# Kernel optimization log

Hardware: AMD Instinct MI355X
Metric: run time of the kernel (lower is better)

Reference implementation:

```python
import jax, jax.numpy as jnp
import numpy as np

B, L, SIZE, BACK, H = 4, 1024, 1024, 512, 16
D = SIZE // H  # head_size = 64


def setup_inputs() -> dict:
    key = jax.random.key(0)
    ks = jax.random.split(key, 18)
    s = 0.02
    return {
        "k": jax.random.normal(ks[0], (B, L, SIZE), jnp.float32),
        "v": jax.random.normal(ks[1], (B, L, SIZE), jnp.float32),
        "q": jax.random.normal(ks[2], (B, L, SIZE), jnp.float32),
        "background": jax.random.normal(ks[3], (B, L, BACK), jnp.float32),
        # weights stored [in, out] (pre-transposed vs torch Linear)
        "Wk": jax.random.normal(ks[4], (SIZE, SIZE), jnp.float32) * s,
        "bk": jnp.zeros((SIZE,), jnp.float32),
        "Wv": jax.random.normal(ks[5], (SIZE, SIZE), jnp.float32) * s,
        "bv": jnp.zeros((SIZE,), jnp.float32),
        "Wq": jax.random.normal(ks[6], (SIZE, SIZE), jnp.float32) * s,
        "bq": jnp.zeros((SIZE,), jnp.float32),
        "Wb": jax.random.normal(ks[7], (BACK, SIZE), jnp.float32) * s,
        "bb": jnp.zeros((SIZE,), jnp.float32),
        "Wo": jax.random.normal(ks[8], (SIZE, SIZE), jnp.float32) * s,
        "bo": jnp.zeros((SIZE,), jnp.float32),
    }


def _heads(x):
    # [B, L, H*D] -> [B, H, L, D]
    b, l, _ = x.shape
    return x.reshape(b, l, H, D).transpose(0, 2, 1, 3)


def reference(k, v, q, background, Wk, bk, Wv, bv, Wq, bq, Wb, bb, Wo, bo):
    kh = _heads(k @ Wk + bk)
    vh = _heads(v @ Wv + bv)
    qh = _heads(q @ Wq + bq) / jnp.sqrt(jnp.asarray(D, k.dtype))
    gh = _heads(background @ Wb + bb)
    scores = jnp.einsum("bhqd,bhkd->bhqk", qh, kh)   # [B,H,Lq,Lk]
    gates = jax.nn.sigmoid(jnp.einsum("bhqd,bhkd->bhqk", qh, gh))
    attn = jax.nn.softmax(scores, axis=-1) * gates    # dropout = identity (eval)
    ctx = jnp.einsum("bhqk,bhkd->bhqd", attn, vh)
    ctx = ctx.transpose(0, 2, 1, 3).reshape(k.shape[0], -1, H * D)
    return ctx @ Wo + bo
```

## Files before the change

### kernel.cpp

```cpp
#include <hip/hip_runtime.h>
#include <cstddef>
#include <cstdint>

typedef __attribute__((ext_vector_type(8))) short s16x8;
typedef __attribute__((ext_vector_type(4))) short s16x4;
typedef __attribute__((ext_vector_type(4))) float f32x4;

#define MFMA(a, b, c) __builtin_amdgcn_mfma_f32_16x16x32_bf16(a, b, c, 0, 0, 0)
#define LOG2E 1.44269504088896f

__device__ __forceinline__ short f2bf(float x) {
    uint32_t u = __float_as_uint(x);
    u = (u + 0x7FFFu + ((u >> 16) & 1u)) >> 16;
    return (short)u;
}

__device__ __forceinline__ void gld16(const void* g, void* l) {
    __builtin_amdgcn_global_load_lds(
        (const __attribute__((address_space(1))) unsigned int*)g,
        (__attribute__((address_space(3))) unsigned int*)l, 16, 0, 0);
}

__device__ __forceinline__ float fexp2(float x) {
#if __has_builtin(__builtin_amdgcn_exp2f)
    return __builtin_amdgcn_exp2f(x);
#else
    return exp2f(x);
#endif
}

__device__ __forceinline__ float frcp(float x) {
#if __has_builtin(__builtin_amdgcn_rcpf)
    return __builtin_amdgcn_rcpf(x);
#else
    return 1.f / x;
#endif
}

__device__ __forceinline__ unsigned cvtpk(float lo, float hi) {
    unsigned r;
    asm("v_cvt_pk_bf16_f32 %0, %1, %2" : "=v"(r) : "v"(lo), "v"(hi));
    return r;
}

struct ConvP { const float* in[4]; short* out[4]; };

__global__ __launch_bounds__(256)
void conv_all(ConvP p) {
    const int i = blockIdx.x * 256 + threadIdx.x;
    int r, base;
    if (i < 524288)            { r = 0; base = 0; }
    else if (i < 1048576)      { r = 1; base = 524288; }
    else if (i < 1310720)      { r = 2; base = 1048576; }
    else                       { r = 3; base = 1310720; }
    const int j = i - base;
    const float4 a = *(const float4*)(p.in[r] + (size_t)j * 8);
    const float4 b = *(const float4*)(p.in[r] + (size_t)j * 8 + 4);
    s16x8 o;
    o[0] = f2bf(a.x); o[1] = f2bf(a.y); o[2] = f2bf(a.z); o[3] = f2bf(a.w);
    o[4] = f2bf(b.x); o[5] = f2bf(b.y); o[6] = f2bf(b.z); o[7] = f2bf(b.w);
    *(s16x8*)(p.out[r] + (size_t)j * 8) = o;
}

struct WtP { const float* W[5]; short* Wt[5]; int K[5]; };

__global__ __launch_bounds__(256)
void conv_wt_b(WtP p) {
    __shared__ float T[64][65];
    const int z = blockIdx.z;
    const int K = p.K[z];
    const int k0 = blockIdx.y << 6, n0 = blockIdx.x << 6;
    if (k0 >= K) return;
    const float* W = p.W[z];
    short* Wt = p.Wt[z];
    const int tr = threadIdx.x >> 4, tc4 = (threadIdx.x & 15) << 2;
    #pragma unroll
    for (int i = 0; i < 4; ++i) {
        const int r = tr + i * 16;
        const float4 v = *(const float4*)(W + (size_t)(k0 + r) * 1024 + n0 + tc4);
        T[r][tc4 + 0] = v.x; T[r][tc4 + 1] = v.y;
        T[r][tc4 + 2] = v.z; T[r][tc4 + 3] = v.w;
    }
    __syncthreads();
    #pragma unroll
    for (int i = 0; i < 4; ++i) {
        const int nr = tr + i * 16;
        s16x4 o;
        o[0] = f2bf(T[tc4 + 0][nr]); o[1] = f2bf(T[tc4 + 1][nr]);
        o[2] = f2bf(T[tc4 + 2][nr]); o[3] = f2bf(T[tc4 + 3][nr]);
        *(s16x4*)(Wt + (size_t)(n0 + nr) * K + k0 + tc4) = o;
    }
}

struct Proj5P {
    const short* A[5]; const short* Bt[5]; const float* bias[5];
    void* Y[5]; int Kd[5]; float alpha[5]; int mode[5];
};

__global__ __launch_bounds__(256, 2)
void proj_gemm128d(Proj5P p, int zbase) {
    __shared__ __align__(16) short lds[2 * 16384];

    const int tid = threadIdx.x;
    const int w = tid >> 6, lane = tid & 63;
    const int la = lane & 15, kg = lane >> 4;
    const int wr = w >> 1, wc = w & 1;

    const int cpx = gridDim.x >> 3;
    const int orig = blockIdx.x;
    const int swz = (orig & 7) * cpx + (orig >> 3);
    const int z = zbase + (swz >> 8);
    const int rem = swz & 255;
    const int bm = rem >> 3, bn = rem & 7;

    const short* __restrict__ A  = p.A[z];
    const short* __restrict__ Bt = p.Bt[z];
    const int K = p.Kd[z];
    const int NT = K >> 6;

    const int srow = tid >> 3;
    const int csrc = (tid & 7) ^ (srow & 7);
    const short* gA = A  + (size_t)(bm * 128 + srow) * K + csrc * 8;
    const short* gB = Bt + (size_t)(bn * 128 + srow) * K + csrc * 8;
    short* dstA = &lds[srow * 64 + (tid & 7) * 8];
    short* dstB = dstA + 8192;

#define STAGE(t, nb) do {                                                  \
        const size_t ko_ = (size_t)((t) << 6);                             \
        short* ba_ = dstA + (nb) * 16384;                                  \
        short* bb_ = dstB + (nb) * 16384;                                  \
        _Pragma("unroll")                                                  \
        for (int i = 0; i < 4; ++i) {                                      \
            gld16(gA + (size_t)(32 * i) * K + ko_, ba_ + i * 2048);        \
            gld16(gB + (size_t)(32 * i) * K + ko_, bb_ + i * 2048);       \
        }                                                                  \
    } while (0)

    const int c0 = kg ^ (la & 7), c1 = (4 + kg) ^ (la & 7);
    const int aRd = (wr * 64 + la) * 64;
    const int bRd = 8192 + (wc * 64 + la) * 64;

    f32x4 acc[4][4] = {};

    STAGE(0, 0);
    asm volatile("s_waitcnt vmcnt(0)" ::: "memory");
    asm volatile("s_barrier" ::: "memory");

    for (int t = 0; t < NT; ++t) {
        const int cb = (t & 1) * 16384;
        if (t + 1 < NT) STAGE(t + 1, (t & 1) ^ 1);
        s16x8 af[4][2], bf[4][2];
        #pragma unroll
        for (int m = 0; m < 4; ++m) {
            af[m][0] = *(const s16x8*)&lds[cb + aRd + m * 1024 + c0 * 8];
            af[m][1] = *(const s16x8*)&lds[cb + aRd + m * 1024 + c1 * 8];
        }
        #pragma unroll
        for (int n = 0; n < 4; ++n) {
            bf[n][0] = *(const s16x8*)&lds[cb + bRd + n * 1024 + c0 * 8];
            bf[n][1] = *(const s16x8*)&lds[cb + bRd + n * 1024 + c1 * 8];
        }
        __builtin_amdgcn_s_setprio(1);
        #pragma unroll
        for (int m = 0; m < 4; ++m)
            #pragma unroll
            for (int n = 0; n < 4; ++n) {
                acc[m][n] = MFMA(af[m][0], bf[n][0], acc[m][n]);
                acc[m][n] = MFMA(af[m][1], bf[n][1], acc[m][n]);
            }
        __builtin_amdgcn_s_setprio(0);
        if (t + 1 < NT) {
            asm volatile("s_waitcnt vmcnt(0)" ::: "memory");
            asm volatile("s_barrier" ::: "memory");
        }
    }
#undef STAGE

    const float* __restrict__ bias = p.bias[z];
    const float alpha = p.alpha[z];
    const int mode = p.mode[z];

    if (mode == 2) {
        short* __restrict__ Y = (short*)p.Y[z];
        short* Tv = lds;
        asm volatile("s_waitcnt lgkmcnt(0)" ::: "memory");
        asm volatile("s_barrier" ::: "memory");
        #pragma unroll
        for (int ni = 0; ni < 4; ++ni) {
            const int rrow = wc * 64 + ni * 16 + la;
            const float bs = bias[bn * 128 + rrow];
            #pragma unroll
            for (int mi = 0; mi < 4; ++mi) {
                const int l0 = wr * 64 + mi * 16 + kg * 4;
                const unsigned d0 = cvtpk(alpha * (acc[mi][ni][0] + bs),
                                          alpha * (acc[mi][ni][1] + bs));
                const unsigned d1 = cvtpk(alpha * (acc[mi][ni][2] + bs),
                                          alpha * (acc[mi][ni][3] + bs));
                *(unsigned*)&Tv[rrow * 132 + l0]     = d0;
                *(unsigned*)&Tv[rrow * 132 + l0 + 2] = d1;
            }
        }
        asm volatile("s_barrier" ::: "memory");
        const int bb_ = (bm * 128) >> 10;
        const int l0g = (bm * 128) & 1023;
        #pragma unroll
        for (int s = 0; s < 8; ++s) {
            const int c = tid + (s << 8);
            const int rr = c >> 4, seg = c & 15;
            const int hh = bn * 2 + (rr >> 6), dd = rr & 63;
            const s16x8 vv = *(const s16x8*)&Tv[rr * 132 + seg * 8];
            *(s16x8*)&Y[((((size_t)bb_ * 16 + hh) * 64 + dd) << 10) + l0g + seg * 8] = vv;
        }
        return;
    }

    #pragma unroll
    for (int n = 0; n < 4; ++n) {
        const int col = bn * 128 + wc * 64 + n * 16 + la;
        const float bs = bias[col];
        #pragma unroll
        for (int m = 0; m < 4; ++m) {
            const int row0 = bm * 128 + wr * 64 + m * 16 + kg * 4;
            #pragma unroll
            for (int r = 0; r < 4; ++r) {
                const float v = alpha * (acc[m][n][r] + bs);
                if (mode == 0) {
                    ((short*)p.Y[z])[(size_t)(row0 + r) * 1024 + col] = f2bf(v);
                } else {
                    ((float*)p.Y[z])[(size_t)(row0 + r) * 1024 + col] = v;
                }
            }
        }
    }
}

__global__ __launch_bounds__(256)
void attn_mfma(const short* __restrict__ qh, const short* __restrict__ kh,
               const short* __restrict__ gh, const short* __restrict__ vt,
               short* __restrict__ ctx) {
    __shared__ __align__(16) short Ks[64 * 64];
    __shared__ __align__(16) short Gs[64 * 64];
    __shared__ __align__(16) short Vs[64 * 64];
    __shared__ __align__(16) short Ps[4][16 * 72];

    const int tid = threadIdx.x, w = tid >> 6, lane = tid & 63;
    const int la = lane & 15, kg = lane >> 4;
    const int q0 = blockIdx.x << 6;
    const int b = blockIdx.y >> 4, h = blockIdx.y & 15;
    const size_t hb = ((size_t)b << 20) + ((size_t)h << 6);
    const size_t vtbase = ((size_t)(b * 16 + h)) << 16;

    const int qrow = q0 + w * 16 + la;
    const s16x8 aq0 = *(const s16x8*)(qh + hb + (size_t)qrow * 1024 + kg * 8);
    const s16x8 aq1 = *(const s16x8*)(qh + hb + (size_t)qrow * 1024 + 32 + kg * 8);

    const int rl = lane >> 3;
    const int cs = (lane & 7) ^ rl;
    const size_t kgoff = hb + (size_t)(w * 8 + rl) * 1024 + cs * 8;
    const size_t vgoff = vtbase + (size_t)(w * 8 + rl) * 1024 + cs * 8;
    short* ldK0 = &Ks[(w * 8) * 64];      short* ldK1 = &Ks[(32 + w * 8) * 64];
    short* ldG0 = &Gs[(w * 8) * 64];      short* ldG1 = &Gs[(32 + w * 8) * 64];
    short* ldV0 = &Vs[(w * 8) * 64];      short* ldV1 = &Vs[(32 + w * 8) * 64];

    const int ch0 = (kg ^ (la & 7)) * 8;
    const int ch1 = ((4 + kg) ^ (la & 7)) * 8;

    float s_run = 0.f;
    f32x4 o[4] = {};

    for (int kt = 0; kt < 16; ++kt) {
        const size_t k0 = (size_t)(kt << 6);
        __syncthreads();
        gld16(kh + kgoff + k0 * 1024, ldK0);
        gld16(kh + kgoff + (k0 + 32) * 1024, ldK1);
        gld16(gh + kgoff + k0 * 1024, ldG0);
        gld16(gh + kgoff + (k0 + 32) * 1024, ldG1);
        gld16(vt + vgoff + k0, ldV0);
        gld16(vt + vgoff + 32 * 1024 + k0, ldV1);
        __syncthreads();

        f32x4 st[4] = {}, gt[4] = {};
        #pragma unroll
        for (int nf = 0; nf < 4; ++nf) {
            const int rb = (nf * 16 + la) * 64;
            const s16x8 kb0 = *(const s16x8*)&Ks[rb + ch0];
            const s16x8 kb1 = *(const s16x8*)&Ks[rb + ch1];
            st[nf] = MFMA(kb0, aq0, st[nf]);
            st[nf] = MFMA(kb1, aq1, st[nf]);
            const s16x8 gb0 = *(const s16x8*)&Gs[rb + ch0];
            const s16x8 gb1 = *(const s16x8*)&Gs[rb + ch1];
            gt[nf] = MFMA(gb0, aq0, gt[nf]);
            gt[nf] = MFMA(gb1, aq1, gt[nf]);
        }

        float ps = 0.f;
        unsigned pkw[4][2];
        #pragma unroll
        for (int nf = 0; nf < 4; ++nf) {
            const float p0 = fexp2(st[nf][0]);
            const float p1 = fexp2(st[nf][1]);
            const float p2 = fexp2(st[nf][2]);
            const float p3 = fexp2(st[nf][3]);
            ps += (p0 + p1) + (p2 + p3);
            const float g0 = frcp(1.f + fexp2(-gt[nf][0]));
            const float g1 = frcp(1.f + fexp2(-gt[nf][1]));
            const float g2 = frcp(1.f + fexp2(-gt[nf][2]));
            const float g3 = frcp(1.f + fexp2(-gt[nf][3]));
            pkw[nf][0] = cvtpk(p0 * g0, p1 * g1);
            pkw[nf][1] = cvtpk(p2 * g2, p3 * g3);
        }
        s_run += ps;

        #pragma unroll
        for (int nf = 0; nf < 4; ++nf) {
            *(unsigned*)&Ps[w][la * 72 + nf * 16 + kg * 4]     = pkw[nf][0];
            *(unsigned*)&Ps[w][la * 72 + nf * 16 + kg * 4 + 2] = pkw[nf][1];
        }

        const s16x8 pa0 = *(const s16x8*)&Ps[w][la * 72 + kg * 8];
        const s16x8 pa1 = *(const s16x8*)&Ps[w][la * 72 + 32 + kg * 8];
        #pragma unroll
        for (int nf = 0; nf < 4; ++nf) {
            const int rb = (nf * 16 + la) * 64;
            const s16x8 vb0 = *(const s16x8*)&Vs[rb + ch0];
            const s16x8 vb1 = *(const s16x8*)&Vs[rb + ch1];
            o[nf] = MFMA(vb0, pa0, o[nf]);
            o[nf] = MFMA(vb1, pa1, o[nf]);
        }
    }

    float sv = s_run;
    sv += __shfl_xor(sv, 16);
    sv += __shfl_xor(sv, 32);
    const float inv = frcp(sv);
    short* crow = ctx + ((size_t)(b * 1024 + qrow) << 10) + (h << 6);
    #pragma unroll
    for (int nf = 0; nf < 4; ++nf) {
        *(unsigned*)(crow + nf * 16 + kg * 4)     = cvtpk(o[nf][0] * inv, o[nf][1] * inv);
        *(unsigned*)(crow + nf * 16 + kg * 4 + 2) = cvtpk(o[nf][2] * inv, o[nf][3] * inv);
    }
}

extern "C" void kernel_launch(void* const* d_in, const int* in_sizes, int n_in,
                              void* d_out, int out_size, void* d_ws, size_t ws_size,
                              hipStream_t stream) {
    (void)in_sizes; (void)n_in; (void)out_size; (void)ws_size;

    const float* k  = (const float*)d_in[0];
    const float* v  = (const float*)d_in[1];
    const float* q  = (const float*)d_in[2];
    const float* bg = (const float*)d_in[3];
    const float* Wk = (const float*)d_in[4];  const float* bk = (const float*)d_in[5];
    const float* Wv = (const float*)d_in[6];  const float* bv = (const float*)d_in[7];
    const float* Wq = (const float*)d_in[8];  const float* bq = (const float*)d_in[9];
    const float* Wb = (const float*)d_in[10]; const float* bb = (const float*)d_in[11];
    const float* Wo = (const float*)d_in[12]; const float* bo = (const float*)d_in[13];

    short* ws = (short*)d_ws;
    const size_t MN = (size_t)4096 * 1024;
    short* khb = ws;
    short* qhb = ws + MN;
    short* ghb = ws + 2 * MN;
    short* vtb = ws + 3 * MN;
    short* xk  = ws + 4 * MN;
    short* xq  = ws + 5 * MN;
    short* xg  = ws + 6 * MN;
    short* xv  = ws + 6 * MN + MN / 2;
    short* wkt = ws + 7 * MN + MN / 2;
    short* wvt = wkt + 1048576;
    short* wqt = wvt + 1048576;
    short* wot = wqt + 1048576;
    short* wbt = wot + 1048576;
    short* ctxb = xk;

    const dim3 blk(256);

    WtP wp;
    wp.W[0] = Wk; wp.Wt[0] = wkt; wp.K[0] = 1024;
    wp.W[1] = Wv; wp.Wt[1] = wvt; wp.K[1] = 1024;
    wp.W[2] = Wq; wp.Wt[2] = wqt; wp.K[2] = 1024;
    wp.W[3] = Wb; wp.Wt[3] = wbt; wp.K[3] = 512;
    wp.W[4] = Wo; wp.Wt[4] = wot; wp.K[4] = 1024;
    conv_wt_b<<<dim3(16, 16, 5), blk, 0, stream>>>(wp);

    ConvP cp;
    cp.in[0] = k;  cp.out[0] = xk;
    cp.in[1] = q;  cp.out[1] = xq;
    cp.in[2] = bg; cp.out[2] = xg;
    cp.in[3] = v;  cp.out[3] = xv;
    conv_all<<<7168, blk, 0, stream>>>(cp);

    Proj5P p5;
    p5.A[0] = xk;   p5.Bt[0] = wkt; p5.bias[0] = bk; p5.Y[0] = khb;
    p5.Kd[0] = 1024; p5.alpha[0] = LOG2E;  p5.mode[0] = 0;
    p5.A[1] = xq;   p5.Bt[1] = wqt; p5.bias[1] = bq; p5.Y[1] = qhb;
    p5.Kd[1] = 1024; p5.alpha[1] = 0.125f; p5.mode[1] = 0;
    p5.A[2] = xg;   p5.Bt[2] = wbt; p5.bias[2] = bb; p5.Y[2] = ghb;
    p5.Kd[2] = 512;  p5.alpha[2] = LOG2E;  p5.mode[2] = 0;
    p5.A[3] = xv;   p5.Bt[3] = wvt; p5.bias[3] = bv; p5.Y[3] = vtb;
    p5.Kd[3] = 1024; p5.alpha[3] = 1.0f;   p5.mode[3] = 2;
    p5.A[4] = ctxb; p5.Bt[4] = wot; p5.bias[4] = bo; p5.Y[4] = d_out;
    p5.Kd[4] = 1024; p5.alpha[4] = 1.0f;   p5.mode[4] = 1;

    proj_gemm128d<<<dim3(1024), blk, 0, stream>>>(p5, 0);

    attn_mfma<<<dim3(16, 64), blk, 0, stream>>>(qhb, khb, ghb, vtb, ctxb);

    proj_gemm128d<<<dim3(256), blk, 0, stream>>>(p5, 4);
}
```

Before: 126.4 us.

## Double-buffer attention K/G/V tiles with 512-thread blocks and XCD-aware mapping

The attention kernel now uses 512-thread blocks that each cover 128 query rows, so every staged K/G/V tile is shared by twice as many waves. K, G and V tiles are double-buffered in one unified LDS array, and the next tile's global-to-LDS loads are issued before the current tile's compute, with one wait and barrier per iteration instead of two syncthreads. Blocks are remapped so each XCD handles contiguous batch-head groups, which should improve L2 locality. The costs are more LDS per block (about 66KB) and lower block-level occupancy.

```diff
diff --git a/kernel.cpp b/kernel.cpp
--- a/kernel.cpp
+++ b/kernel.cpp
@@ -234,61 +234,68 @@
     }
 }
 
-__global__ __launch_bounds__(256)
+__global__ __launch_bounds__(512)
 void attn_mfma(const short* __restrict__ qh, const short* __restrict__ kh,
                const short* __restrict__ gh, const short* __restrict__ vt,
                short* __restrict__ ctx) {
-    __shared__ __align__(16) short Ks[64 * 64];
-    __shared__ __align__(16) short Gs[64 * 64];
-    __shared__ __align__(16) short Vs[64 * 64];
-    __shared__ __align__(16) short Ps[4][16 * 72];
+    __shared__ __align__(16) short lds[33792];
 
     const int tid = threadIdx.x, w = tid >> 6, lane = tid & 63;
     const int la = lane & 15, kg = lane >> 4;
-    const int q0 = blockIdx.x << 6;
-    const int b = blockIdx.y >> 4, h = blockIdx.y & 15;
+
+    const int orig = blockIdx.x;
+    const int xcd = orig & 7, i = orig >> 3;
+    const int bh = xcd * 8 + (i >> 3);
+    const int qt = i & 7;
+    const int b = bh >> 4, h = bh & 15;
+    const int q0 = qt << 7;
+
     const size_t hb = ((size_t)b << 20) + ((size_t)h << 6);
-    const size_t vtbase = ((size_t)(b * 16 + h)) << 16;
+    const size_t vtbase = ((size_t)bh) << 16;
 
     const int qrow = q0 + w * 16 + la;
     const s16x8 aq0 = *(const s16x8*)(qh + hb + (size_t)qrow * 1024 + kg * 8);
     const s16x8 aq1 = *(const s16x8*)(qh + hb + (size_t)qrow * 1024 + 32 + kg * 8);
 
-    const int rl = lane >> 3;
-    const int cs = (lane & 7) ^ rl;
-    const size_t kgoff = hb + (size_t)(w * 8 + rl) * 1024 + cs * 8;
-    const size_t vgoff = vtbase + (size_t)(w * 8 + rl) * 1024 + cs * 8;
-    short* ldK0 = &Ks[(w * 8) * 64];      short* ldK1 = &Ks[(32 + w * 8) * 64];
-    short* ldG0 = &Gs[(w * 8) * 64];      short* ldG1 = &Gs[(32 + w * 8) * 64];
-    short* ldV0 = &Vs[(w * 8) * 64];      short* ldV1 = &Vs[(32 + w * 8) * 64];
+    const int sr = tid >> 3, sc = tid & 7;
+    const int cs = sc ^ (sr & 7);
+    const short* ksrc = kh + hb + (size_t)sr * 1024 + cs * 8;
+    const short* gsrc = gh + hb + (size_t)sr * 1024 + cs * 8;
+    const short* vsrc = vt + vtbase + (size_t)sr * 1024 + cs * 8;
+    const int sdst = tid * 8;
 
     const int ch0 = (kg ^ (la & 7)) * 8;
     const int ch1 = ((4 + kg) ^ (la & 7)) * 8;
+    const int pbase = 24576 + w * 1152;
 
     float s_run = 0.f;
     f32x4 o[4] = {};
 
+#define ASTG(kt, bb) do {                                                  \
+        const size_t kr_ = (size_t)((kt) << 6) * 1024;                     \
+        gld16(ksrc + kr_, &lds[(bb) * 4096 + sdst]);                       \
+        gld16(gsrc + kr_, &lds[8192 + (bb) * 4096 + sdst]);                \
+        gld16(vsrc + ((kt) << 6), &lds[16384 + (bb) * 4096 + sdst]);       \
+    } while (0)
+
+    ASTG(0, 0);
+    asm volatile("s_waitcnt vmcnt(0)" ::: "memory");
+    asm volatile("s_barrier" ::: "memory");
+
     for (int kt = 0; kt < 16; ++kt) {
-        const size_t k0 = (size_t)(kt << 6);
-        __syncthreads();
-        gld16(kh + kgoff + k0 * 1024, ldK0);
-        gld16(kh + kgoff + (k0 + 32) * 1024, ldK1);
-        gld16(gh + kgoff + k0 * 1024, ldG0);
-        gld16(gh + kgoff + (k0 + 32) * 1024, ldG1);
-        gld16(vt + vgoff + k0, ldV0);
-        gld16(vt + vgoff + 32 * 1024 + k0, ldV1);
-        __syncthreads();
+        const int cb = (kt & 1) * 4096;
+        if (kt < 15) ASTG(kt + 1, (kt + 1) & 1);
 
         f32x4 st[4] = {}, gt[4] = {};
         #pragma unroll
         for (int nf = 0; nf < 4; ++nf) {
-            const int rb = (nf * 16 + la) * 64;
-            const s16x8 kb0 = *(const s16x8*)&Ks[rb + ch0];
-            const s16x8 kb1 = *(const s16x8*)&Ks[rb + ch1];
+            const int rb = cb + (nf * 16 + la) * 64;
+            const s16x8 kb0 = *(const s16x8*)&lds[rb + ch0];
+            const s16x8 kb1 = *(const s16x8*)&lds[rb + ch1];
             st[nf] = MFMA(kb0, aq0, st[nf]);
             st[nf] = MFMA(kb1, aq1, st[nf]);
-            const s16x8 gb0 = *(const s16x8*)&Gs[rb + ch0];
-            const s16x8 gb1 = *(const s16x8*)&Gs[rb + ch1];
+            const s16x8 gb0 = *(const s16x8*)&lds[8192 + rb + ch0];
+            const s16x8 gb1 = *(const s16x8*)&lds[8192 + rb + ch1];
             gt[nf] = MFMA(gb0, aq0, gt[nf]);
             gt[nf] = MFMA(gb1, aq1, gt[nf]);
         }
@@ -313,21 +320,27 @@
 
         #pragma unroll
         for (int nf = 0; nf < 4; ++nf) {
-            *(unsigned*)&Ps[w][la * 72 + nf * 16 + kg * 4]     = pkw[nf][0];
-            *(unsigned*)&Ps[w][la * 72 + nf * 16 + kg * 4 + 2] = pkw[nf][1];
-        }
-
-        const s16x8 pa0 = *(const s16x8*)&Ps[w][la * 72 + kg * 8];
-        const s16x8 pa1 = *(const s16x8*)&Ps[w][la * 72 + 32 + kg * 8];
+            *(unsigned*)&lds[pbase + la * 72 + nf * 16 + kg * 4]     = pkw[nf][0];
+            *(unsigned*)&lds[pbase + la * 72 + nf * 16 + kg * 4 + 2] = pkw[nf][1];
+        }
+
+        const s16x8 pa0 = *(const s16x8*)&lds[pbase + la * 72 + kg * 8];
+        const s16x8 pa1 = *(const s16x8*)&lds[pbase + la * 72 + 32 + kg * 8];
         #pragma unroll
         for (int nf = 0; nf < 4; ++nf) {
-            const int rb = (nf * 16 + la) * 64;
-            const s16x8 vb0 = *(const s16x8*)&Vs[rb + ch0];
-            const s16x8 vb1 = *(const s16x8*)&Vs[rb + ch1];
+            const int rb = cb + (nf * 16 + la) * 64;
+            const s16x8 vb0 = *(const s16x8*)&lds[16384 + rb + ch0];
+            const s16x8 vb1 = *(const s16x8*)&lds[16384 + rb + ch1];
             o[nf] = MFMA(vb0, pa0, o[nf]);
             o[nf] = MFMA(vb1, pa1, o[nf]);
         }
-    }
+
+        if (kt < 15) {
+            asm volatile("s_waitcnt vmcnt(0)" ::: "memory");
+            asm volatile("s_barrier" ::: "memory");
+        }
+    }
+#undef ASTG
 
     float sv = s_run;
     sv += __shfl_xor(sv, 16);
@@ -404,7 +417,7 @@
 
     proj_gemm128d<<<dim3(1024), blk, 0, stream>>>(p5, 0);
 
-    attn_mfma<<<dim3(16, 64), blk, 0, stream>>>(qhb, khb, ghb, vtb, ctxb);
+    attn_mfma<<<dim3(512), dim3(512), 0, stream>>>(qhb, khb, ghb, vtb, ctxb);
 
     proj_gemm128d<<<dim3(256), blk, 0, stream>>>(p5, 4);
 }
```

After: 118.6 us. 1.07x faster.
